# Optimization experiments

Hardware: AMD Instinct MI355X
Metric: run time of the kernel (lower is better)

## Reference

```python
import jax, jax.numpy as jnp
import numpy as np

HEADS = 8
EPS = 1e-5


def setup_inputs() -> dict:
    key = jax.random.key(0)
    ks = jax.random.split(key, 4)
    B, S, N, C = 1, 192, 256, 256
    msa = jax.random.normal(ks[0], (B, S, N, C), dtype=jnp.float32)
    w_qkv = jax.random.normal(ks[1], (3 * C, C), dtype=jnp.float32) * 0.02
    b_qkv = jnp.zeros((3 * C,), dtype=jnp.float32)
    w_out = jax.random.normal(ks[2], (C, C), dtype=jnp.float32) * 0.02
    b_out = jnp.zeros((C,), dtype=jnp.float32)
    gamma = jnp.ones((C,), dtype=jnp.float32)
    beta = jnp.zeros((C,), dtype=jnp.float32)
    return {"msa": msa, "w_qkv": w_qkv, "b_qkv": b_qkv, "w_out": w_out,
            "b_out": b_out, "gamma": gamma, "beta": beta}


def reference(msa, w_qkv, b_qkv, w_out, b_out, gamma, beta):
    B, S, N, C = msa.shape
    H = HEADS
    D = C // H
    scale = D ** -0.5
    # column attention: attend over the S (MSA depth) axis per residue n
    msa_t = jnp.transpose(msa, (0, 2, 1, 3))                 # [B,N,S,C]
    qkv = msa_t @ w_qkv.T + b_qkv                             # [B,N,S,3C]
    qkv = qkv.reshape(B, N, S, 3, H, D)
    q, k, v = qkv[..., 0, :, :], qkv[..., 1, :, :], qkv[..., 2, :, :]  # [B,N,S,H,D]
    attn = jnp.einsum('bnshd,bnthd->bnhst', q, k) * scale     # [B,N,H,S,S]
    attn = jax.nn.softmax(attn, axis=-1)
    out = jnp.einsum('bnhst,bnthd->bnshd', attn, v).reshape(B, N, S, C)
    out = jnp.transpose(out, (0, 2, 1, 3))                    # [B,S,N,C]
    out = out @ w_out.T + b_out
    x = msa + out
    mu = jnp.mean(x, axis=-1, keepdims=True)
    var = jnp.mean(jnp.square(x - mu), axis=-1, keepdims=True)
    return (x - mu) * jax.lax.rsqrt(var + EPS) * gamma + beta
```

## Files before the change

kernel.cpp:

```cpp
#include <hip/hip_runtime.h>
#include <stdint.h>

#define S_DIM 192
#define N_DIM 256
#define C_DIM 256
#define H_DIM 8
#define D_DIM 32
#define QKV_STRIDE (N_DIM * H_DIM * S_DIM * D_DIM)

typedef float f32x4 __attribute__((ext_vector_type(4)));
typedef float f32x16 __attribute__((ext_vector_type(16)));
typedef short bf16x8 __attribute__((ext_vector_type(8)));

__device__ __forceinline__ unsigned short f2bf(float f) {
  union { float f; unsigned u; } v; v.f = f;
  unsigned r = v.u + 0x7FFFu + ((v.u >> 16) & 1u);
  return (unsigned short)(r >> 16);
}

__device__ __forceinline__ unsigned cvt_pk_bf16(float lo, float hi) {
  unsigned r;
  asm("v_cvt_pk_bf16_f32 %0, %1, %2" : "=v"(r) : "v"(lo), "v"(hi));
  return r;
}

__device__ __forceinline__ void gl2lds16(const void* g, void* l) {
  __builtin_amdgcn_global_load_lds(
      (const __attribute__((address_space(1))) unsigned int*)g,
      (__attribute__((address_space(3))) unsigned int*)l, 16, 0, 0);
}

__global__ __launch_bounds__(256) void k_prep(const float* __restrict__ msa,
                                              unsigned short* __restrict__ A,
                                              const float* __restrict__ wq,
                                              const float* __restrict__ wo,
                                              unsigned short* __restrict__ dq,
                                              unsigned short* __restrict__ do_) {
  int b = blockIdx.x;
  if (b < 12288) {
    int tid = b * 256 + threadIdx.x;
    int token = tid >> 6;
    int c4 = tid & 63;
    int n = token / S_DIM;
    int s = token - n * S_DIM;
    float4 v = *(const float4*)(msa + ((size_t)(s * N_DIM + n) << 8) + (c4 << 2));
    ushort4 o;
    o.x = f2bf(v.x); o.y = f2bf(v.y); o.z = f2bf(v.z); o.w = f2bf(v.w);
    *(ushort4*)(A + ((size_t)token << 8) + (c4 << 2)) = o;
  } else {
    int tid = (b - 12288) * 256 + threadIdx.x;
    const float* src; unsigned short* dst; int idx;
    if (tid < 49152) { src = wq; dst = dq; idx = tid; }
    else { src = wo; dst = do_; idx = tid - 49152; }
    float4 v = *(const float4*)(src + (size_t)idx * 4);
    ushort4 o;
    o.x = f2bf(v.x); o.y = f2bf(v.y); o.z = f2bf(v.z); o.w = f2bf(v.w);
    *(ushort4*)(dst + (size_t)idx * 4) = o;
  }
}

__global__ __launch_bounds__(512) void k_qkv(const unsigned short* __restrict__ A,
                                             const unsigned short* __restrict__ W,
                                             const float* __restrict__ bq,
                                             unsigned short* __restrict__ qkv) {
  __shared__ unsigned short As[256 * 64];
  __shared__ unsigned short Bs[128 * 64];
  const int tid = threadIdx.x;
  const int lane = tid & 63, wid = tid >> 6;
  const int l16 = lane & 15, lg = lane >> 4;
  const int wr = wid >> 1, wc = wid & 1;
  const int bm0 = blockIdx.x * 256;
  const int bn0 = blockIdx.y * 128;
  const int lrow = lane >> 3, lchunk = lane & 7;
  const int sw = ((lchunk ^ lrow) * 8);

  f32x4 acc[4][4] = {};

  for (int ks = 0; ks < 4; ks++) {
    const int k0 = ks * 64;
    __syncthreads();
#pragma unroll
    for (int q = 0; q < 4; q++) {
      int base_row = wid * 32 + q * 8;
      gl2lds16(A + (size_t)(bm0 + base_row + lrow) * 256 + k0 + sw, &As[base_row * 64]);
    }
#pragma unroll
    for (int q = 0; q < 2; q++) {
      int base_row = wid * 16 + q * 8;
      gl2lds16(W + (size_t)(bn0 + base_row + lrow) * 256 + k0 + sw, &Bs[base_row * 64]);
    }
    __syncthreads();
#pragma unroll
    for (int kk = 0; kk < 2; kk++) {
      const int xr = ((kk * 4 + lg) ^ (l16 & 7)) * 8;
      bf16x8 a[4], b[4];
#pragma unroll
      for (int m = 0; m < 4; m++)
        a[m] = *(const bf16x8*)&As[(wr * 64 + m * 16 + l16) * 64 + xr];
#pragma unroll
      for (int n2 = 0; n2 < 4; n2++)
        b[n2] = *(const bf16x8*)&Bs[(wc * 64 + n2 * 16 + l16) * 64 + xr];
      if (bn0 < 512) {
#pragma unroll
        for (int m = 0; m < 4; m++)
#pragma unroll
          for (int n2 = 0; n2 < 4; n2++)
            acc[m][n2] = __builtin_amdgcn_mfma_f32_16x16x32_bf16(b[n2], a[m], acc[m][n2], 0, 0, 0);
      } else {
#pragma unroll
        for (int m = 0; m < 4; m++)
#pragma unroll
          for (int n2 = 0; n2 < 4; n2++)
            acc[m][n2] = __builtin_amdgcn_mfma_f32_16x16x32_bf16(a[m], b[n2], acc[m][n2], 0, 0, 0);
      }
    }
  }

  const int t3 = bn0 >> 8;
  if (t3 < 2) {
#pragma unroll
    for (int n2 = 0; n2 < 4; n2++) {
      int j0 = bn0 + wc * 64 + n2 * 16 + lg * 4;
      float4 b4 = *(const float4*)&bq[j0];
      int c0 = j0 & 255;
      int h = c0 >> 5, d0 = c0 & 31;
#pragma unroll
      for (int m = 0; m < 4; m++) {
        int token = bm0 + wr * 64 + m * 16 + l16;
        int n = token / S_DIM;
        int s = token - n * S_DIM;
        ushort4 o;
        o.x = f2bf(acc[m][n2][0] + b4.x);
        o.y = f2bf(acc[m][n2][1] + b4.y);
        o.z = f2bf(acc[m][n2][2] + b4.z);
        o.w = f2bf(acc[m][n2][3] + b4.w);
        *(ushort4*)(qkv + (size_t)t3 * QKV_STRIDE +
                    ((size_t)((n * 8 + h) * 192 + s)) * 32 + d0) = o;
      }
    }
  } else {
#pragma unroll
    for (int n2 = 0; n2 < 4; n2++) {
      int j = bn0 + wc * 64 + n2 * 16 + l16;
      int hd = j - 512;
      int h = hd >> 5, d = hd & 31;
      float bias = bq[j];
#pragma unroll
      for (int m = 0; m < 4; m++) {
        int t0 = bm0 + wr * 64 + m * 16 + lg * 4;
        int n = t0 / S_DIM;
        int s0 = t0 - n * S_DIM;
        ushort4 o;
        o.x = f2bf(acc[m][n2][0] + bias);
        o.y = f2bf(acc[m][n2][1] + bias);
        o.z = f2bf(acc[m][n2][2] + bias);
        o.w = f2bf(acc[m][n2][3] + bias);
        *(ushort4*)(qkv + (size_t)2 * QKV_STRIDE + ((size_t)(n * 8 + h) * 32 + d) * 192 + s0) = o;
      }
    }
  }
}

__global__ __launch_bounds__(384) void k_attn2(const unsigned short* __restrict__ qkv,
                                               unsigned short* __restrict__ attn_out) {
  const int lane = threadIdx.x & 63;
  const int l32 = lane & 31;
  const int hi = lane >> 5;
  const int qt = threadIdx.x >> 6;
  const int nh = blockIdx.x;
  const int n = nh >> 3, h = nh & 7;
  const unsigned short* Qp = qkv + (size_t)nh * (192 * 32);
  const unsigned short* Kp = qkv + (size_t)QKV_STRIDE + (size_t)nh * (192 * 32);
  const unsigned short* Vt = qkv + (size_t)2 * QKV_STRIDE + (size_t)nh * (32 * 192);
  const int q0 = qt * 32;

  bf16x8 bq0 = *(const bf16x8*)(Qp + (q0 + l32) * 32 + hi * 8);
  bf16x8 bq1 = *(const bf16x8*)(Qp + (q0 + l32) * 32 + 16 + hi * 8);

  f32x16 accO = {};
  float m_run = -1e30f, l_run = 0.f;
  const float scale = 0.17677669529663687f;
  const float DEFER = 8.0f / 0.17677669529663687f;

  bf16x8 ka0 = *(const bf16x8*)(Kp + l32 * 32 + hi * 8);
  bf16x8 ka1 = *(const bf16x8*)(Kp + l32 * 32 + 16 + hi * 8);

  for (int t = 0; t < 6; t++) {
    bf16x8 kn0, kn1;
    if (t < 5) {
      kn0 = *(const bf16x8*)(Kp + ((t + 1) * 32 + l32) * 32 + hi * 8);
      kn1 = *(const bf16x8*)(Kp + ((t + 1) * 32 + l32) * 32 + 16 + hi * 8);
    }
    f32x16 sv = {};
    sv = __builtin_amdgcn_mfma_f32_32x32x16_bf16(ka0, bq0, sv, 0, 0, 0);
    sv = __builtin_amdgcn_mfma_f32_32x32x16_bf16(ka1, bq1, sv, 0, 0, 0);

    bf16x8 bv0 = *(const bf16x8*)(Vt + (size_t)l32 * 192 + t * 32 + hi * 8);
    bf16x8 bv1 = *(const bf16x8*)(Vt + (size_t)l32 * 192 + t * 32 + 16 + hi * 8);

    float tmx = sv[0];
#pragma unroll
    for (int r = 1; r < 16; r++) tmx = fmaxf(tmx, sv[r]);
    tmx = fmaxf(tmx, __shfl_xor(tmx, 32));

    bool need = tmx > m_run + DEFER;
    if (__ballot(need)) {
      float m_new = fmaxf(m_run, tmx);
      float corr = __expf((m_run - m_new) * scale);
      l_run *= corr;
#pragma unroll
      for (int r = 0; r < 16; r++) {
        int qr = (r & 3) + 8 * (r >> 2) + 4 * hi;
        accO[r] *= __shfl(corr, qr);
      }
      m_run = m_new;
    }

    float ssum = 0.f;
#pragma unroll
    for (int r = 0; r < 16; r++) {
      float p2 = __expf((sv[r] - m_run) * scale);
      sv[r] = p2;
      ssum += p2;
    }
    ssum += __shfl_xor(ssum, 32);
    l_run += ssum;

    unsigned pk[8];
#pragma unroll
    for (int g = 0; g < 4; g++) {
      pk[2 * g]     = cvt_pk_bf16(sv[4 * g],     sv[4 * g + 1]);
      pk[2 * g + 1] = cvt_pk_bf16(sv[4 * g + 2], sv[4 * g + 3]);
    }

#pragma unroll
    for (int kh = 0; kh < 2; kh++) {
      unsigned sa = hi ? pk[4 * kh]     : pk[4 * kh + 2];
      unsigned sb = hi ? pk[4 * kh + 1] : pk[4 * kh + 3];
      unsigned pa = __shfl_xor((int)sa, 32);
      unsigned pb = __shfl_xor((int)sb, 32);
      union { unsigned u[4]; bf16x8 v; } af;
      af.u[0] = hi ? pa : pk[4 * kh];
      af.u[1] = hi ? pb : pk[4 * kh + 1];
      af.u[2] = hi ? pk[4 * kh + 2] : pa;
      af.u[3] = hi ? pk[4 * kh + 3] : pb;
      accO = __builtin_amdgcn_mfma_f32_32x32x16_bf16(af.v, kh ? bv1 : bv0, accO, 0, 0, 0);
    }
    ka0 = kn0; ka1 = kn1;
  }

  float inv = 1.0f / l_run;
#pragma unroll
  for (int r = 0; r < 16; r++) {
    int qr = (r & 3) + 8 * (r >> 2) + 4 * hi;
    float v = accO[r] * __shfl(inv, qr);
    attn_out[((size_t)((q0 + qr) * 256 + n)) * 256 + h * 32 + l32] = f2bf(v);
  }
}

__global__ __launch_bounds__(256) void k_out(const unsigned short* __restrict__ Aat,
                                             const unsigned short* __restrict__ W,
                                             const float* __restrict__ bo,
                                             const float* __restrict__ msa,
                                             const float* __restrict__ gamma,
                                             const float* __restrict__ beta,
                                             float* __restrict__ out) {
  __shared__ unsigned short As[128 * 64];
  __shared__ unsigned short Bs[256 * 64];
  const int tid = threadIdx.x;
  const int lane = tid & 63, wid = tid >> 6;
  const int l16 = lane & 15, lg = lane >> 4;
  const int bm0 = blockIdx.x * 128;
  const int lrow = lane >> 3, lchunk = lane & 7;
  const int sw = ((lchunk ^ lrow) * 8);

  f32x4 acc[2][16] = {};

  for (int ks = 0; ks < 4; ks++) {
    const int k0 = ks * 64;
    __syncthreads();
#pragma unroll
    for (int q = 0; q < 4; q++) {
      int base_row = wid * 32 + q * 8;
      gl2lds16(Aat + (size_t)(bm0 + base_row + lrow) * 256 + k0 + sw, &As[base_row * 64]);
    }
#pragma unroll
    for (int q = 0; q < 8; q++) {
      int base_row = wid * 64 + q * 8;
      gl2lds16(W + (size_t)(base_row + lrow) * 256 + k0 + sw, &Bs[base_row * 64]);
    }
    __syncthreads();
#pragma unroll
    for (int kk = 0; kk < 2; kk++) {
      const int xr = ((kk * 4 + lg) ^ (l16 & 7)) * 8;
      bf16x8 a[2];
#pragma unroll
      for (int m = 0; m < 2; m++)
        a[m] = *(const bf16x8*)&As[(wid * 32 + m * 16 + l16) * 64 + xr];
#pragma unroll
      for (int c = 0; c < 16; c++) {
        bf16x8 b = *(const bf16x8*)&Bs[(c * 16 + l16) * 64 + xr];
#pragma unroll
        for (int m = 0; m < 2; m++)
          acc[m][c] = __builtin_amdgcn_mfma_f32_16x16x32_bf16(a[m], b, acc[m][c], 0, 0, 0);
      }
    }
  }

#pragma unroll
  for (int m = 0; m < 2; m++) {
#pragma unroll
    for (int c = 0; c < 16; c++) {
      int col = c * 16 + l16;
      float bias = bo[col];
#pragma unroll
      for (int i = 0; i < 4; i++) {
        int row = bm0 + wid * 32 + m * 16 + lg * 4 + i;
        acc[m][c][i] += bias + msa[(size_t)row * 256 + col];
      }
    }
#pragma unroll
    for (int i = 0; i < 4; i++) {
      float s1 = 0.f, s2 = 0.f;
#pragma unroll
      for (int c = 0; c < 16; c++) { float x = acc[m][c][i]; s1 += x; s2 += x * x; }
      s1 += __shfl_xor(s1, 1); s2 += __shfl_xor(s2, 1);
      s1 += __shfl_xor(s1, 2); s2 += __shfl_xor(s2, 2);
      s1 += __shfl_xor(s1, 4); s2 += __shfl_xor(s2, 4);
      s1 += __shfl_xor(s1, 8); s2 += __shfl_xor(s2, 8);
      float mu = s1 * (1.0f / 256.0f);
      float var = s2 * (1.0f / 256.0f) - mu * mu;
      float rstd = rsqrtf(var + 1e-5f);
      int row = bm0 + wid * 32 + m * 16 + lg * 4 + i;
#pragma unroll
      for (int c = 0; c < 16; c++) {
        int col = c * 16 + l16;
        float y = (acc[m][c][i] - mu) * rstd * gamma[col] + beta[col];
        out[(size_t)row * 256 + col] = y;
      }
    }
  }
}

extern "C" void kernel_launch(void* const* d_in, const int* in_sizes, int n_in,
                              void* d_out, int out_size, void* d_ws, size_t ws_size,
                              hipStream_t stream) {
  const float* msa   = (const float*)d_in[0];
  const float* w_qkv = (const float*)d_in[1];
  const float* b_qkv = (const float*)d_in[2];
  const float* w_out = (const float*)d_in[3];
  const float* b_out = (const float*)d_in[4];
  const float* gamma = (const float*)d_in[5];
  const float* beta  = (const float*)d_in[6];
  float* out = (float*)d_out;

  char* ws = (char*)d_ws;
  unsigned short* A      = (unsigned short*)(ws);
  unsigned short* qkvbuf = (unsigned short*)(ws + 25165824ull);
  unsigned short* wq_bf  = (unsigned short*)(ws + 4ull * 25165824ull);
  unsigned short* wo_bf  = (unsigned short*)(ws + 4ull * 25165824ull + 393216ull);

  k_prep<<<12544, 256, 0, stream>>>(msa, A, w_qkv, w_out, wq_bf, wo_bf);
  dim3 g2(192, 6);
  k_qkv<<<g2, 512, 0, stream>>>(A, wq_bf, b_qkv, qkvbuf);
  k_attn2<<<2048, 384, 0, stream>>>(qkvbuf, A);
  k_out<<<384, 256, 0, stream>>>(A, wo_bf, b_out, msa, gamma, beta, out);
}
```

Baseline: 135.9 us.

## Fuse msa transpose and bf16 conversion into QKV GEMM A-tile loads

Removes the separate prep pass that transposed and converted the full msa tensor to bf16. The QKV GEMM now loads fp32 msa rows directly, converts them in registers and writes them swizzled into LDS. The GEMM tile is halved to 128x128 with 256 threads, and a remapped 1D grid raster is added for locality. This saves the write and re-read of a large intermediate, but each A-tile load now moves fp32 data through registers, strided across tokens, instead of using direct global-to-LDS copies.

```diff
diff --git a/kernel.cpp b/kernel.cpp
--- a/kernel.cpp
+++ b/kernel.cpp
@@ -30,63 +30,65 @@
       (__attribute__((address_space(3))) unsigned int*)l, 16, 0, 0);
 }
 
-__global__ __launch_bounds__(256) void k_prep(const float* __restrict__ msa,
-                                              unsigned short* __restrict__ A,
-                                              const float* __restrict__ wq,
+__global__ __launch_bounds__(256) void k_cvt2(const float* __restrict__ wq,
                                               const float* __restrict__ wo,
                                               unsigned short* __restrict__ dq,
                                               unsigned short* __restrict__ do_) {
-  int b = blockIdx.x;
-  if (b < 12288) {
-    int tid = b * 256 + threadIdx.x;
-    int token = tid >> 6;
-    int c4 = tid & 63;
-    int n = token / S_DIM;
-    int s = token - n * S_DIM;
-    float4 v = *(const float4*)(msa + ((size_t)(s * N_DIM + n) << 8) + (c4 << 2));
-    ushort4 o;
-    o.x = f2bf(v.x); o.y = f2bf(v.y); o.z = f2bf(v.z); o.w = f2bf(v.w);
-    *(ushort4*)(A + ((size_t)token << 8) + (c4 << 2)) = o;
-  } else {
-    int tid = (b - 12288) * 256 + threadIdx.x;
-    const float* src; unsigned short* dst; int idx;
-    if (tid < 49152) { src = wq; dst = dq; idx = tid; }
-    else { src = wo; dst = do_; idx = tid - 49152; }
-    float4 v = *(const float4*)(src + (size_t)idx * 4);
-    ushort4 o;
-    o.x = f2bf(v.x); o.y = f2bf(v.y); o.z = f2bf(v.z); o.w = f2bf(v.w);
-    *(ushort4*)(dst + (size_t)idx * 4) = o;
-  }
-}
-
-__global__ __launch_bounds__(512) void k_qkv(const unsigned short* __restrict__ A,
+  int tid = blockIdx.x * 256 + threadIdx.x;
+  const float* src; unsigned short* dst; int idx;
+  if (tid < 49152) { src = wq; dst = dq; idx = tid; }
+  else { src = wo; dst = do_; idx = tid - 49152; }
+  float4 v = *(const float4*)(src + (size_t)idx * 4);
+  ushort4 o;
+  o.x = f2bf(v.x); o.y = f2bf(v.y); o.z = f2bf(v.z); o.w = f2bf(v.w);
+  *(ushort4*)(dst + (size_t)idx * 4) = o;
+}
+
+__global__ __launch_bounds__(256) void k_qkv(const float* __restrict__ msa,
                                              const unsigned short* __restrict__ W,
                                              const float* __restrict__ bq,
                                              unsigned short* __restrict__ qkv) {
-  __shared__ unsigned short As[256 * 64];
+  __shared__ unsigned short As[128 * 64];
   __shared__ unsigned short Bs[128 * 64];
   const int tid = threadIdx.x;
   const int lane = tid & 63, wid = tid >> 6;
   const int l16 = lane & 15, lg = lane >> 4;
   const int wr = wid >> 1, wc = wid & 1;
-  const int bm0 = blockIdx.x * 256;
-  const int bn0 = blockIdx.y * 128;
+  const int p = blockIdx.x;
+  const int o = (p & 7) * 288 + (p >> 3);
+  const int bm0 = (o / 6) * 128;
+  const int bn0 = (o % 6) * 128;
   const int lrow = lane >> 3, lchunk = lane & 7;
   const int sw = ((lchunk ^ lrow) * 8);
+  const int arow16 = tid >> 4;
+  const int ac = tid & 15;
 
   f32x4 acc[4][4] = {};
 
   for (int ks = 0; ks < 4; ks++) {
     const int k0 = ks * 64;
+    float4 av[8];
+#pragma unroll
+    for (int p2 = 0; p2 < 8; p2++) {
+      int r = p2 * 16 + arow16;
+      int token = bm0 + r;
+      int nn = token / S_DIM;
+      int ss = token - nn * S_DIM;
+      av[p2] = *(const float4*)(msa + ((size_t)(ss * 256 + nn)) * 256 + k0 + ac * 4);
+    }
     __syncthreads();
+#pragma unroll
+    for (int p2 = 0; p2 < 8; p2++) {
+      int r = p2 * 16 + arow16;
+      uint2 u;
+      u.x = cvt_pk_bf16(av[p2].x, av[p2].y);
+      u.y = cvt_pk_bf16(av[p2].z, av[p2].w);
+      int cc = ac >> 1, half = ac & 1;
+      *(uint2*)((char*)As + r * 128 + ((cc ^ (r & 7)) * 16) + half * 8) = u;
+    }
 #pragma unroll
     for (int q = 0; q < 4; q++) {
       int base_row = wid * 32 + q * 8;
-      gl2lds16(A + (size_t)(bm0 + base_row + lrow) * 256 + k0 + sw, &As[base_row * 64]);
-    }
-#pragma unroll
-    for (int q = 0; q < 2; q++) {
-      int base_row = wid * 16 + q * 8;
       gl2lds16(W + (size_t)(bn0 + base_row + lrow) * 256 + k0 + sw, &Bs[base_row * 64]);
     }
     __syncthreads();
@@ -129,13 +131,13 @@
         int token = bm0 + wr * 64 + m * 16 + l16;
         int n = token / S_DIM;
         int s = token - n * S_DIM;
-        ushort4 o;
-        o.x = f2bf(acc[m][n2][0] + b4.x);
-        o.y = f2bf(acc[m][n2][1] + b4.y);
-        o.z = f2bf(acc[m][n2][2] + b4.z);
-        o.w = f2bf(acc[m][n2][3] + b4.w);
+        ushort4 o2;
+        o2.x = f2bf(acc[m][n2][0] + b4.x);
+        o2.y = f2bf(acc[m][n2][1] + b4.y);
+        o2.z = f2bf(acc[m][n2][2] + b4.z);
+        o2.w = f2bf(acc[m][n2][3] + b4.w);
         *(ushort4*)(qkv + (size_t)t3 * QKV_STRIDE +
-                    ((size_t)((n * 8 + h) * 192 + s)) * 32 + d0) = o;
+                    ((size_t)((n * 8 + h) * 192 + s)) * 32 + d0) = o2;
       }
     }
   } else {
@@ -150,12 +152,12 @@
         int t0 = bm0 + wr * 64 + m * 16 + lg * 4;
         int n = t0 / S_DIM;
         int s0 = t0 - n * S_DIM;
-        ushort4 o;
-        o.x = f2bf(acc[m][n2][0] + bias);
-        o.y = f2bf(acc[m][n2][1] + bias);
-        o.z = f2bf(acc[m][n2][2] + bias);
-        o.w = f2bf(acc[m][n2][3] + bias);
-        *(ushort4*)(qkv + (size_t)2 * QKV_STRIDE + ((size_t)(n * 8 + h) * 32 + d) * 192 + s0) = o;
+        ushort4 o2;
+        o2.x = f2bf(acc[m][n2][0] + bias);
+        o2.y = f2bf(acc[m][n2][1] + bias);
+        o2.z = f2bf(acc[m][n2][2] + bias);
+        o2.w = f2bf(acc[m][n2][3] + bias);
+        *(ushort4*)(qkv + (size_t)2 * QKV_STRIDE + ((size_t)(n * 8 + h) * 32 + d) * 192 + s0) = o2;
       }
     }
   }
@@ -355,14 +357,13 @@
   float* out = (float*)d_out;
 
   char* ws = (char*)d_ws;
-  unsigned short* A      = (unsigned short*)(ws);
-  unsigned short* qkvbuf = (unsigned short*)(ws + 25165824ull);
-  unsigned short* wq_bf  = (unsigned short*)(ws + 4ull * 25165824ull);
-  unsigned short* wo_bf  = (unsigned short*)(ws + 4ull * 25165824ull + 393216ull);
-
-  k_prep<<<12544, 256, 0, stream>>>(msa, A, w_qkv, w_out, wq_bf, wo_bf);
-  dim3 g2(192, 6);
-  k_qkv<<<g2, 512, 0, stream>>>(A, wq_bf, b_qkv, qkvbuf);
-  k_attn2<<<2048, 384, 0, stream>>>(qkvbuf, A);
-  k_out<<<384, 256, 0, stream>>>(A, wo_bf, b_out, msa, gamma, beta, out);
-}
+  unsigned short* qkvbuf = (unsigned short*)(ws);
+  unsigned short* attn   = (unsigned short*)(ws + 75497472ull);
+  unsigned short* wq_bf  = (unsigned short*)(ws + 75497472ull + 25165824ull);
+  unsigned short* wo_bf  = (unsigned short*)(ws + 75497472ull + 25165824ull + 393216ull);
+
+  k_cvt2<<<256, 256, 0, stream>>>(w_qkv, w_out, wq_bf, wo_bf);
+  k_qkv<<<2304, 256, 0, stream>>>(msa, wq_bf, b_qkv, qkvbuf);
+  k_attn2<<<2048, 384, 0, stream>>>(qkvbuf, attn);
+  k_out<<<384, 256, 0, stream>>>(attn, wo_bf, b_out, msa, gamma, beta, out);
+}
```

Result: faster. 127.3 us (-6.3%).
